# Performance work log

Hardware: AMD Instinct MI355X
Metric: run time of the kernel (lower is better)

## Reference

```python
import jax, jax.numpy as jnp
import numpy as np

N_NODES = 50000
N_EDGES = 800000
NODE_IN = 5
EDGE_IN = 1
HID = 64


def setup_inputs() -> dict:
    key = jax.random.key(0)
    ks = jax.random.split(key, 16)
    x = jax.random.normal(ks[0], (N_NODES, NODE_IN), dtype=jnp.float32)
    edge_index = jax.random.randint(ks[1], (2, N_EDGES), 0, N_NODES, dtype=jnp.int32)
    edge_attr = jax.random.normal(ks[2], (N_EDGES, EDGE_IN), dtype=jnp.float32)
    def lin(k, fan_in, fan_out):
        b = 1.0 / np.sqrt(fan_in)
        k1, k2 = jax.random.split(k)
        W = jax.random.uniform(k1, (fan_in, fan_out), minval=-b, maxval=b, dtype=jnp.float32)
        bi = jax.random.uniform(k2, (fan_out,), minval=-b, maxval=b, dtype=jnp.float32)
        return W, bi
    W_ne, b_ne = lin(ks[3], NODE_IN, HID)
    W_ee, b_ee = lin(ks[4], EDGE_IN, HID)
    W_gcn, b_gcn = lin(ks[5], HID, HID)   # PyG GCNConv: lin (no bias) + separate bias
    W1, b1 = lin(ks[6], 3 * HID, HID)
    W2, b2 = lin(ks[7], HID, 1)
    return {"x": x, "edge_index": edge_index, "edge_attr": edge_attr,
            "W_ne": W_ne, "b_ne": b_ne, "W_ee": W_ee, "b_ee": b_ee,
            "W_gcn": W_gcn, "b_gcn": b_gcn, "W1": W1, "b1": b1, "W2": W2, "b2": b2}


def gcn_conv(h, edge_index, W, b):
    # PyG GCNConv: add self-loops, symmetric norm D^-1/2 (A+I) D^-1/2, linear, scatter-add.
    N = h.shape[0]
    src, dst = edge_index[0], edge_index[1]
    loops = jnp.arange(N, dtype=src.dtype)
    row = jnp.concatenate([src, loops])  # message sources
    col = jnp.concatenate([dst, loops])  # message targets
    deg = jax.ops.segment_sum(jnp.ones(col.shape[0], h.dtype), col, num_segments=N)
    dinv = jnp.where(deg > 0, jax.lax.rsqrt(deg), 0.0)
    norm = dinv[row] * dinv[col]          # [E+N]
    ht = h @ W                            # [N, HID]
    msg = ht[row] * norm[:, None]         # gather + scale
    return jax.ops.segment_sum(msg, col, num_segments=N) + b


def reference(x, edge_index, edge_attr, W_ne, b_ne, W_ee, b_ee, W_gcn, b_gcn, W1, b1, W2, b2):
    h = jax.nn.relu(x @ W_ne + b_ne)                    # node encoder
    ef = jax.nn.relu(edge_attr @ W_ee + b_ee)           # edge encoder
    h = gcn_conv(h, edge_index, W_gcn, b_gcn)           # GCN layer
    src, dst = edge_index[0], edge_index[1]
    edge_input = jnp.concatenate([h[src], h[dst], ef], axis=1)  # [E, 3*HID]
    out = jax.nn.relu(edge_input @ W1 + b1) @ W2 + b2   # edge MLP -> [E, 1]
    return out.reshape(-1)
```

## Files before the change

kernel.cpp:

```cpp
#include <hip/hip_runtime.h>

#define NN 50000
#define NE 800000
#define H  64
#define NBKT 196
#define BCAP 8192
#define BIN_CHUNK 2048

typedef __attribute__((ext_vector_type(8))) short bf16x8;
typedef __attribute__((ext_vector_type(4))) float f32x4;

__device__ __forceinline__ unsigned short f2bf(float f) {
  unsigned int u = __builtin_bit_cast(unsigned int, f);
  u += 0x7FFFu + ((u >> 16) & 1u);
  return (unsigned short)(u >> 16);
}
__device__ __forceinline__ float bf2f(unsigned short u) {
  unsigned int v = ((unsigned int)u) << 16;
  return __builtin_bit_cast(float, v);
}

__global__ __launch_bounds__(256) void k_prep(
    const float* __restrict__ W1, const float* __restrict__ b1,
    const float* __restrict__ W_ee, const float* __restrict__ b_ee,
    float* __restrict__ thrS, float* __restrict__ cT,
    unsigned short* __restrict__ w1f, int* __restrict__ gcur) {
  const int t = threadIdx.x;
  if (blockIdx.x == 2) {
    if (t < NBKT) gcur[t] = 0;
    return;
  }
  if (blockIdx.x == 1) {
    const int ln = t & 63, q = t >> 6;
    const int l15_ = ln & 15, l4_ = ln >> 4;
#pragma unroll
    for (int f = 0; f < 4; ++f) {
      const int idx = q * 4 + f;
      const int g = idx >> 3;
      const int ct = (idx >> 1) & 3;
      const int c = idx & 1;
#pragma unroll
      for (int j = 0; j < 8; ++j) {
        const int k = g * 64 + c * 32 + l4_ * 8 + j;
        const int hcol = ct * 16 + l15_;
        w1f[(idx * 64 + ln) * 8 + j] = f2bf(W1[k * H + hcol]);
      }
    }
    return;
  }
  __shared__ float swee[64], sbee[64], sth[64];
  __shared__ int skx[64];
  if (t < 64) {
    const float w = W_ee[t], b = b_ee[t];
    swee[t] = w; sbee[t] = b;
    sth[t] = (w != 0.f) ? (-b / w) : __builtin_inff();
    skx[t] = t;
  }
  __syncthreads();
  for (int sz = 2; sz <= 64; sz <<= 1)
    for (int st = sz >> 1; st > 0; st >>= 1) {
      if (t < 64) {
        const int p = t ^ st;
        if (p > t) {
          const bool up = ((t & sz) == 0);
          const float a = sth[t], bb = sth[p];
          if (up ? (a > bb) : (a < bb)) {
            const int ka = skx[t];
            sth[t] = bb; sth[p] = a;
            skx[t] = skx[p]; skx[p] = ka;
          }
        }
      }
      __syncthreads();
    }
  if (t < 64) {
    const int h = t;
    float c1 = 0.f, c0 = b1[h];
    for (int k = 0; k < 64; ++k) {
      const float w = swee[k], b = sbee[k];
      if (w < 0.f || (w == 0.f && b > 0.f)) {
        const float wv1 = W1[(128 + k) * H + h];
        c1 = fmaf(w, wv1, c1);
        c0 = fmaf(b, wv1, c0);
      }
    }
    float2* cT2 = (float2*)cT;
    cT2[h] = make_float2(c1, c0);
    for (int iv = 1; iv <= 64; ++iv) {
      const int ks = skx[iv - 1];
      const float w = swee[ks];
      const float s = (w > 0.f) ? 1.f : -1.f;
      const float wv1 = W1[(128 + ks) * H + h];
      c1 = fmaf(s * w, wv1, c1);
      c0 = fmaf(s * sbee[ks], wv1, c0);
      cT2[iv * 66 + h] = make_float2(c1, c0);
    }
    thrS[h] = sth[h];
  }
}

__global__ __launch_bounds__(256) void k_bin(const int* __restrict__ ei,
                                             unsigned int* __restrict__ gbin,
                                             int* __restrict__ gcur) {
  __shared__ int hist[NBKT], base[NBKT];
  const int t = threadIdx.x;
  if (t < NBKT) hist[t] = 0;
  __syncthreads();

  const int e0 = blockIdx.x * BIN_CHUNK;
  int srcv[8], dstv[8], loff[8];
#pragma unroll
  for (int j = 0; j < 8; ++j) {
    const int e = e0 + j * 256 + t;
    if (e < NE) {
      srcv[j] = ei[e];
      dstv[j] = ei[NE + e];
      loff[j] = atomicAdd(&hist[dstv[j] >> 8], 1);
    } else dstv[j] = -1;
  }
  __syncthreads();
  if (t < NBKT) base[t] = atomicAdd(&gcur[t], hist[t]);
  __syncthreads();
#pragma unroll
  for (int j = 0; j < 8; ++j) {
    if (dstv[j] >= 0) {
      const int b = dstv[j] >> 8;
      const int pos = base[b] + loff[j];
      if (pos < BCAP)
        gbin[(size_t)b * BCAP + pos] =
            ((unsigned int)srcv[j] << 8) | (unsigned int)(dstv[j] & 255);
    }
  }
}

__global__ __launch_bounds__(256) void k_pass2(const unsigned int* __restrict__ gbin,
                                               const int* __restrict__ gcur,
                                               unsigned short* __restrict__ gcsr,
                                               int2* __restrict__ rowrange,
                                               float* __restrict__ dinv) {
  __shared__ int hist[256], cur[256], sc[256];
  __shared__ unsigned short lcsr[BCAP];
  const int b = blockIdx.x, t = threadIdx.x;
  const int sz = min(gcur[b], BCAP);
  hist[t] = 0;
  __syncthreads();

  const unsigned int* bb = gbin + (size_t)b * BCAP;
  for (int i = t; i < sz; i += 256) atomicAdd(&hist[bb[i] & 255], 1);
  __syncthreads();

  int v = hist[t];
  const int cnt = v;
  sc[t] = v;
  __syncthreads();
#pragma unroll
  for (int off = 1; off < 256; off <<= 1) {
    const int o = (t >= off) ? sc[t - off] : 0;
    __syncthreads();
    v += o;
    sc[t] = v;
    __syncthreads();
  }
  const int ex = v - cnt;
  cur[t] = ex;
  const int d = b * 256 + t;
  if (d < NN) {
    const int beg = b * BCAP + ex;
    rowrange[d] = make_int2(beg, beg + cnt);
    dinv[d] = rsqrtf((float)(cnt + 1));
  }
  __syncthreads();

  for (int i = t; i < sz; i += 256) {
    const unsigned int en = bb[i];
    const int off = atomicAdd(&cur[en & 255], 1);
    lcsr[off] = (unsigned short)(en >> 8);
  }
  __syncthreads();
  for (int i = t; i < sz; i += 256) gcsr[(size_t)b * BCAP + i] = lcsr[i];
}

__global__ __launch_bounds__(256) void k_node(
    const float* __restrict__ x, const float* __restrict__ W_ne,
    const float* __restrict__ b_ne, const float* __restrict__ W_gcn,
    const float* __restrict__ dinv, unsigned short* __restrict__ htb) {
  __shared__ float sh[4][H];
  const int lane = threadIdx.x & 63;
  const int wv   = threadIdx.x >> 6;
  const int n    = blockIdx.x * 4 + wv;

  float acc = b_ne[lane];
#pragma unroll
  for (int k = 0; k < 5; ++k) acc = fmaf(x[n * 5 + k], W_ne[k * H + lane], acc);
  acc = fmaxf(acc, 0.0f);
  sh[wv][lane] = acc;
  __syncthreads();

  float hv = 0.0f;
#pragma unroll 8
  for (int k = 0; k < H; ++k) hv = fmaf(sh[wv][k], W_gcn[k * H + lane], hv);

  htb[(size_t)n * H + lane] = f2bf(hv * dinv[n]);
}

__global__ __launch_bounds__(256) void k_gather_uv(
    const int2* __restrict__ rowrange, const unsigned short* __restrict__ gcsr,
    const unsigned short* __restrict__ htb, const float* __restrict__ dinv,
    const float* __restrict__ b_gcn, const unsigned short* __restrict__ w1f,
    unsigned short* __restrict__ u, unsigned short* __restrict__ v) {
  __shared__ unsigned short shg[16 * 64];
  const int lane = threadIdx.x & 63;
  const int wv   = threadIdx.x >> 6;
  const int n0   = blockIdx.x * 16;
  const float bg = b_gcn[lane];

#pragma unroll 1
  for (int q = 0; q < 4; ++q) {
    const int nl = wv * 4 + q;
    const int n  = n0 + nl;
    const int2 rr = rowrange[n];
    float sum = bf2f(htb[(size_t)n * H + lane]);
    int i = rr.x;
#pragma unroll 1
    for (; i + 4 <= rr.y; i += 4) {
      const int s0 = gcsr[i], s1 = gcsr[i + 1];
      const int s2 = gcsr[i + 2], s3 = gcsr[i + 3];
      const float v0 = bf2f(htb[(size_t)s0 * H + lane]);
      const float v1 = bf2f(htb[(size_t)s1 * H + lane]);
      const float v2 = bf2f(htb[(size_t)s2 * H + lane]);
      const float v3 = bf2f(htb[(size_t)s3 * H + lane]);
      sum += (v0 + v1) + (v2 + v3);
    }
#pragma unroll 1
    for (; i < rr.y; ++i) sum += bf2f(htb[(size_t)gcsr[i] * H + lane]);

    const float hgv = fmaf(dinv[n], sum, bg);
    shg[((nl * 128 + lane * 2) ^ ((nl & 7) << 4)) >> 1] = f2bf(hgv);
  }
  __syncthreads();

  const int l15 = lane & 15, l4 = lane >> 4;
  const bf16x8 a0 = *(const bf16x8*)(shg + (((l15 * 128 + l4 * 16) ^ ((l15 & 7) << 4)) >> 1));
  const bf16x8 a1 = *(const bf16x8*)(shg + (((l15 * 128 + 64 + l4 * 16) ^ ((l15 & 7) << 4)) >> 1));

  const int ct = wv;
  const bf16x8 bu0 = *(const bf16x8*)(w1f + ((ct * 2 + 0) * 64 + lane) * 8);
  const bf16x8 bu1 = *(const bf16x8*)(w1f + ((ct * 2 + 1) * 64 + lane) * 8);
  const bf16x8 bv0 = *(const bf16x8*)(w1f + ((8 + ct * 2 + 0) * 64 + lane) * 8);
  const bf16x8 bv1 = *(const bf16x8*)(w1f + ((8 + ct * 2 + 1) * 64 + lane) * 8);

  f32x4 au = (f32x4)(0.f), av = (f32x4)(0.f);
  au = __builtin_amdgcn_mfma_f32_16x16x32_bf16(a0, bu0, au, 0, 0, 0);
  au = __builtin_amdgcn_mfma_f32_16x16x32_bf16(a1, bu1, au, 0, 0, 0);
  av = __builtin_amdgcn_mfma_f32_16x16x32_bf16(a0, bv0, av, 0, 0, 0);
  av = __builtin_amdgcn_mfma_f32_16x16x32_bf16(a1, bv1, av, 0, 0, 0);

#pragma unroll
  for (int r = 0; r < 4; ++r) {
    const size_t idx = (size_t)(n0 + l4 * 4 + r) * H + ct * 16 + l15;
    u[idx] = f2bf(au[r]);
    v[idx] = f2bf(av[r]);
  }
}

__device__ __forceinline__ int find_iv(const float* __restrict__ sThr, float ea) {
  int iv = 0;
#pragma unroll
  for (int st = 64; st >= 1; st >>= 1) {
    const int nc = iv + st;
    if (nc <= 64 && sThr[nc - 1] <= ea) iv = nc;
  }
  return iv;
}

__device__ __forceinline__ void edge_compute(
    float ea, uint4 U0, uint4 U1, uint4 V0, uint4 V1,
    const float* __restrict__ sThr, const float* __restrict__ sCT,
    const float* __restrict__ w2v, int l4, int lane, float b2v,
    float* __restrict__ out, int obase) {
  const int iv = find_iv(sThr, ea);
  const float* cp = sCT + iv * 132 + l4 * 32;
  const unsigned int ud[8] = {U0.x, U0.y, U0.z, U0.w, U1.x, U1.y, U1.z, U1.w};
  const unsigned int vd[8] = {V0.x, V0.y, V0.z, V0.w, V1.x, V1.y, V1.z, V1.w};
  float p = 0.f;
#pragma unroll
  for (int r = 0; r < 8; ++r) {
    const float4 cc = *(const float4*)(cp + r * 4);
    const float ulo = __builtin_bit_cast(float, ud[r] << 16);
    const float uhi = __builtin_bit_cast(float, ud[r] & 0xFFFF0000u);
    const float vlo = __builtin_bit_cast(float, vd[r] << 16);
    const float vhi = __builtin_bit_cast(float, vd[r] & 0xFFFF0000u);
    const float z0 = ulo + vlo + fmaf(ea, cc.x, cc.y);
    const float z1 = uhi + vhi + fmaf(ea, cc.z, cc.w);
    p = fmaf(fmaxf(z0, 0.f), w2v[2 * r], p);
    p = fmaf(fmaxf(z1, 0.f), w2v[2 * r + 1], p);
  }
  p += __shfl_xor(p, 16);
  p += __shfl_xor(p, 32);
  if (lane < 16) out[obase + lane] = p + b2v;
}

#define ET 5
__global__ __launch_bounds__(256) void k_edge(
    const int* __restrict__ ei, const float* __restrict__ eattr,
    const unsigned short* __restrict__ u, const unsigned short* __restrict__ v,
    const float* __restrict__ thrS, const float* __restrict__ cT,
    const float* __restrict__ W2, const float* __restrict__ b2,
    float* __restrict__ out) {
  __shared__ float sThr[64];
  __shared__ float sCT[65 * 132];

  const int t = threadIdx.x;
  if (t < 64) sThr[t] = thrS[t];
  for (int i = t; i < 65 * 66; i += 256)
    ((float2*)sCT)[i] = ((const float2*)cT)[i];
  __syncthreads();

  const int lane = t & 63;
  const int wv   = t >> 6;
  const int l15  = lane & 15, l4 = lane >> 4;
  const float b2v = b2[0];

  float w2v[16];
#pragma unroll
  for (int j = 0; j < 16; ++j) w2v[j] = W2[l4 * 16 + j];

  const int tile0 = (blockIdx.x * 4 + wv) * ET;
  int srcA[ET], dstA[ET];
  float eaA[ET];
#pragma unroll
  for (int tt = 0; tt < ET; ++tt) {
    srcA[tt] = ei[(tile0 + tt) * 16 + l15];
    dstA[tt] = ei[NE + (tile0 + tt) * 16 + l15];
    eaA[tt]  = eattr[(tile0 + tt) * 16 + l15];
  }

  uint4 Au0, Au1, Av0, Av1, Bu0, Bu1, Bv0, Bv1;

#define LOADUV(U0, U1, V0, V1, tt) {                              \
    const unsigned short* up = u + (size_t)srcA[tt] * H + l4 * 16; \
    const unsigned short* vp = v + (size_t)dstA[tt] * H + l4 * 16; \
    U0 = *(const uint4*)(up); U1 = *(const uint4*)(up + 8);        \
    V0 = *(const uint4*)(vp); V1 = *(const uint4*)(vp + 8); }

  LOADUV(Au0, Au1, Av0, Av1, 0);
  LOADUV(Bu0, Bu1, Bv0, Bv1, 1);
  edge_compute(eaA[0], Au0, Au1, Av0, Av1, sThr, sCT, w2v, l4, lane, b2v, out, (tile0 + 0) * 16);
  LOADUV(Au0, Au1, Av0, Av1, 2);
  edge_compute(eaA[1], Bu0, Bu1, Bv0, Bv1, sThr, sCT, w2v, l4, lane, b2v, out, (tile0 + 1) * 16);
  LOADUV(Bu0, Bu1, Bv0, Bv1, 3);
  edge_compute(eaA[2], Au0, Au1, Av0, Av1, sThr, sCT, w2v, l4, lane, b2v, out, (tile0 + 2) * 16);
  LOADUV(Au0, Au1, Av0, Av1, 4);
  edge_compute(eaA[3], Bu0, Bu1, Bv0, Bv1, sThr, sCT, w2v, l4, lane, b2v, out, (tile0 + 3) * 16);
  edge_compute(eaA[4], Au0, Au1, Av0, Av1, sThr, sCT, w2v, l4, lane, b2v, out, (tile0 + 4) * 16);
#undef LOADUV
}

extern "C" void kernel_launch(void* const* d_in, const int* in_sizes, int n_in,
                              void* d_out, int out_size, void* d_ws, size_t ws_size,
                              hipStream_t stream) {
  const float* x     = (const float*)d_in[0];
  const int*   ei    = (const int*)d_in[1];
  const float* eattr = (const float*)d_in[2];
  const float* W_ne  = (const float*)d_in[3];
  const float* b_ne  = (const float*)d_in[4];
  const float* W_ee  = (const float*)d_in[5];
  const float* b_ee  = (const float*)d_in[6];
  const float* W_gcn = (const float*)d_in[7];
  const float* b_gcn = (const float*)d_in[8];
  const float* W1    = (const float*)d_in[9];
  const float* b1    = (const float*)d_in[10];
  const float* W2    = (const float*)d_in[11];
  const float* b2    = (const float*)d_in[12];
  float* out = (float*)d_out;

  char* ws = (char*)d_ws;
  unsigned short* htb = (unsigned short*)(ws + 0);
  unsigned short* uT  = (unsigned short*)(ws + 6400000);
  unsigned int*   gbin = (unsigned int*)(ws + 12800000);
  unsigned short* vT  = (unsigned short*)(ws + 12800000);
  unsigned short* gcsr = (unsigned short*)(ws + 19222528);
  int2*  rowrange = (int2*)(ws + 22433792);
  float* dinv    = (float*)(ws + 22833792);
  int*   gcur    = (int*)(ws + 23033792);
  float* thrS    = (float*)(ws + 23034592);
  float* cT      = (float*)(ws + 23034848);
  unsigned short* w1f = (unsigned short*)(ws + 23069168);

  k_prep<<<3, 256, 0, stream>>>(W1, b1, W_ee, b_ee, thrS, cT, w1f, gcur);
  k_bin<<<(NE + BIN_CHUNK - 1) / BIN_CHUNK, 256, 0, stream>>>(ei, gbin, gcur);
  k_pass2<<<NBKT, 256, 0, stream>>>(gbin, gcur, gcsr, rowrange, dinv);
  k_node<<<NN / 4, 256, 0, stream>>>(x, W_ne, b_ne, W_gcn, dinv, htb);
  k_gather_uv<<<NN / 16, 256, 0, stream>>>(rowrange, gcsr, htb, dinv, b_gcn, w1f, uT, vT);
  k_edge<<<NE / (4 * ET * 16), 256, 0, stream>>>(ei, eattr, uT, vT, thrS, cT, W2, b2, out);
}
```

Baseline: 159.4 us.

## Replace CSR build and gather with bucket-wise LDS atomic aggregation

Removes the per-bucket CSR sorting kernel. Node degrees are now counted with global atomics during binning. The gather kernel is replaced by one 1024-thread block per destination bucket, which scatter-adds neighbour features into a shared-memory accumulator with LDS float atomics and then runs the W1 MFMA projection on the 256 rows it owns. This cuts one kernel launch and the CSR write/read traffic. In exchange it adds global atomic contention, uses only 196 large blocks with a large LDS footprint that limits occupancy, and still overlays the v output on the bin buffer.

```diff
diff --git a/kernel.cpp b/kernel.cpp
--- a/kernel.cpp
+++ b/kernel.cpp
@@ -24,10 +24,13 @@
     const float* __restrict__ W1, const float* __restrict__ b1,
     const float* __restrict__ W_ee, const float* __restrict__ b_ee,
     float* __restrict__ thrS, float* __restrict__ cT,
-    unsigned short* __restrict__ w1f, int* __restrict__ gcur) {
+    unsigned short* __restrict__ w1f, int* __restrict__ cnt,
+    int* __restrict__ gcur) {
   const int t = threadIdx.x;
-  if (blockIdx.x == 2) {
-    if (t < NBKT) gcur[t] = 0;
+  if (blockIdx.x >= 2) {
+    const int i = (blockIdx.x - 2) * 256 + t;
+    if (i < NN) cnt[i] = 0;
+    if (blockIdx.x == 2 && t < NBKT) gcur[t] = 0;
     return;
   }
   if (blockIdx.x == 1) {
@@ -101,7 +104,8 @@
 
 __global__ __launch_bounds__(256) void k_bin(const int* __restrict__ ei,
                                              unsigned int* __restrict__ gbin,
-                                             int* __restrict__ gcur) {
+                                             int* __restrict__ gcur,
+                                             int* __restrict__ cnt) {
   __shared__ int hist[NBKT], base[NBKT];
   const int t = threadIdx.x;
   if (t < NBKT) hist[t] = 0;
@@ -116,6 +120,7 @@
       srcv[j] = ei[e];
       dstv[j] = ei[NE + e];
       loff[j] = atomicAdd(&hist[dstv[j] >> 8], 1);
+      atomicAdd(&cnt[dstv[j]], 1);
     } else dstv[j] = -1;
   }
   __syncthreads();
@@ -133,57 +138,10 @@
   }
 }
 
-__global__ __launch_bounds__(256) void k_pass2(const unsigned int* __restrict__ gbin,
-                                               const int* __restrict__ gcur,
-                                               unsigned short* __restrict__ gcsr,
-                                               int2* __restrict__ rowrange,
-                                               float* __restrict__ dinv) {
-  __shared__ int hist[256], cur[256], sc[256];
-  __shared__ unsigned short lcsr[BCAP];
-  const int b = blockIdx.x, t = threadIdx.x;
-  const int sz = min(gcur[b], BCAP);
-  hist[t] = 0;
-  __syncthreads();
-
-  const unsigned int* bb = gbin + (size_t)b * BCAP;
-  for (int i = t; i < sz; i += 256) atomicAdd(&hist[bb[i] & 255], 1);
-  __syncthreads();
-
-  int v = hist[t];
-  const int cnt = v;
-  sc[t] = v;
-  __syncthreads();
-#pragma unroll
-  for (int off = 1; off < 256; off <<= 1) {
-    const int o = (t >= off) ? sc[t - off] : 0;
-    __syncthreads();
-    v += o;
-    sc[t] = v;
-    __syncthreads();
-  }
-  const int ex = v - cnt;
-  cur[t] = ex;
-  const int d = b * 256 + t;
-  if (d < NN) {
-    const int beg = b * BCAP + ex;
-    rowrange[d] = make_int2(beg, beg + cnt);
-    dinv[d] = rsqrtf((float)(cnt + 1));
-  }
-  __syncthreads();
-
-  for (int i = t; i < sz; i += 256) {
-    const unsigned int en = bb[i];
-    const int off = atomicAdd(&cur[en & 255], 1);
-    lcsr[off] = (unsigned short)(en >> 8);
-  }
-  __syncthreads();
-  for (int i = t; i < sz; i += 256) gcsr[(size_t)b * BCAP + i] = lcsr[i];
-}
-
 __global__ __launch_bounds__(256) void k_node(
     const float* __restrict__ x, const float* __restrict__ W_ne,
     const float* __restrict__ b_ne, const float* __restrict__ W_gcn,
-    const float* __restrict__ dinv, unsigned short* __restrict__ htb) {
+    const int* __restrict__ cnt, unsigned short* __restrict__ htb) {
   __shared__ float sh[4][H];
   const int lane = threadIdx.x & 63;
   const int wv   = threadIdx.x >> 6;
@@ -200,66 +158,79 @@
 #pragma unroll 8
   for (int k = 0; k < H; ++k) hv = fmaf(sh[wv][k], W_gcn[k * H + lane], hv);
 
-  htb[(size_t)n * H + lane] = f2bf(hv * dinv[n]);
-}
-
-__global__ __launch_bounds__(256) void k_gather_uv(
-    const int2* __restrict__ rowrange, const unsigned short* __restrict__ gcsr,
-    const unsigned short* __restrict__ htb, const float* __restrict__ dinv,
+  const float dv = rsqrtf((float)(cnt[n] + 1));
+  htb[(size_t)n * H + lane] = f2bf(hv * dv);
+}
+
+__global__ __launch_bounds__(1024) void k_agg(
+    const unsigned int* __restrict__ gbin, const int* __restrict__ gcur,
+    const int* __restrict__ cnt, const unsigned short* __restrict__ htb,
     const float* __restrict__ b_gcn, const unsigned short* __restrict__ w1f,
     unsigned short* __restrict__ u, unsigned short* __restrict__ v) {
-  __shared__ unsigned short shg[16 * 64];
-  const int lane = threadIdx.x & 63;
-  const int wv   = threadIdx.x >> 6;
-  const int n0   = blockIdx.x * 16;
-  const float bg = b_gcn[lane];
-
-#pragma unroll 1
-  for (int q = 0; q < 4; ++q) {
-    const int nl = wv * 4 + q;
-    const int n  = n0 + nl;
-    const int2 rr = rowrange[n];
-    float sum = bf2f(htb[(size_t)n * H + lane]);
-    int i = rr.x;
-#pragma unroll 1
-    for (; i + 4 <= rr.y; i += 4) {
-      const int s0 = gcsr[i], s1 = gcsr[i + 1];
-      const int s2 = gcsr[i + 2], s3 = gcsr[i + 3];
-      const float v0 = bf2f(htb[(size_t)s0 * H + lane]);
-      const float v1 = bf2f(htb[(size_t)s1 * H + lane]);
-      const float v2 = bf2f(htb[(size_t)s2 * H + lane]);
-      const float v3 = bf2f(htb[(size_t)s3 * H + lane]);
-      sum += (v0 + v1) + (v2 + v3);
-    }
-#pragma unroll 1
-    for (; i < rr.y; ++i) sum += bf2f(htb[(size_t)gcsr[i] * H + lane]);
-
-    const float hgv = fmaf(dinv[n], sum, bg);
-    shg[((nl * 128 + lane * 2) ^ ((nl & 7) << 4)) >> 1] = f2bf(hgv);
+  __shared__ float sacc[256 * 66];
+  const int b = blockIdx.x;
+  const int t = threadIdx.x;
+  const int lane = t & 63, wv = t >> 6;
+
+#pragma unroll
+  for (int i = 0; i < 16; ++i) {
+    const int r = wv + i * 16;
+    const int d = b * 256 + r;
+    sacc[r * 66 + lane] = (d < NN) ? bf2f(htb[(size_t)d * H + lane]) : 0.f;
+  }
+  __syncthreads();
+
+  const int sz = min(gcur[b], BCAP);
+  const unsigned int* bb = gbin + (size_t)b * BCAP;
+  int i = wv;
+  for (; i + 16 < sz; i += 32) {
+    const unsigned int e0 = bb[i], e1 = bb[i + 16];
+    const float h0 = bf2f(htb[(size_t)(e0 >> 8) * H + lane]);
+    const float h1 = bf2f(htb[(size_t)(e1 >> 8) * H + lane]);
+    atomicAdd(&sacc[(int)(e0 & 255) * 66 + lane], h0);
+    atomicAdd(&sacc[(int)(e1 & 255) * 66 + lane], h1);
+  }
+  if (i < sz) {
+    const unsigned int e0 = bb[i];
+    const float h0 = bf2f(htb[(size_t)(e0 >> 8) * H + lane]);
+    atomicAdd(&sacc[(int)(e0 & 255) * 66 + lane], h0);
   }
   __syncthreads();
 
   const int l15 = lane & 15, l4 = lane >> 4;
-  const bf16x8 a0 = *(const bf16x8*)(shg + (((l15 * 128 + l4 * 16) ^ ((l15 & 7) << 4)) >> 1));
-  const bf16x8 a1 = *(const bf16x8*)(shg + (((l15 * 128 + 64 + l4 * 16) ^ ((l15 & 7) << 4)) >> 1));
-
-  const int ct = wv;
-  const bf16x8 bu0 = *(const bf16x8*)(w1f + ((ct * 2 + 0) * 64 + lane) * 8);
-  const bf16x8 bu1 = *(const bf16x8*)(w1f + ((ct * 2 + 1) * 64 + lane) * 8);
-  const bf16x8 bv0 = *(const bf16x8*)(w1f + ((8 + ct * 2 + 0) * 64 + lane) * 8);
-  const bf16x8 bv1 = *(const bf16x8*)(w1f + ((8 + ct * 2 + 1) * 64 + lane) * 8);
-
-  f32x4 au = (f32x4)(0.f), av = (f32x4)(0.f);
-  au = __builtin_amdgcn_mfma_f32_16x16x32_bf16(a0, bu0, au, 0, 0, 0);
-  au = __builtin_amdgcn_mfma_f32_16x16x32_bf16(a1, bu1, au, 0, 0, 0);
-  av = __builtin_amdgcn_mfma_f32_16x16x32_bf16(a0, bv0, av, 0, 0, 0);
-  av = __builtin_amdgcn_mfma_f32_16x16x32_bf16(a1, bv1, av, 0, 0, 0);
-
-#pragma unroll
-  for (int r = 0; r < 4; ++r) {
-    const size_t idx = (size_t)(n0 + l4 * 4 + r) * H + ct * 16 + l15;
-    u[idx] = f2bf(au[r]);
-    v[idx] = f2bf(av[r]);
+  const int rowl = wv * 16 + l15;
+  const int nA = b * 256 + rowl;
+  const float dv = (nA < NN) ? rsqrtf((float)(cnt[nA] + 1)) : 0.f;
+
+  bf16x8 a0, a1;
+#pragma unroll
+  for (int j = 0; j < 8; ++j) {
+    a0[j] = (short)f2bf(fmaf(dv, sacc[rowl * 66 + l4 * 8 + j], b_gcn[l4 * 8 + j]));
+    a1[j] = (short)f2bf(fmaf(dv, sacc[rowl * 66 + 32 + l4 * 8 + j], b_gcn[32 + l4 * 8 + j]));
+  }
+
+#pragma unroll
+  for (int ct = 0; ct < 4; ++ct) {
+    const bf16x8 bu0 = *(const bf16x8*)(w1f + ((ct * 2 + 0) * 64 + lane) * 8);
+    const bf16x8 bu1 = *(const bf16x8*)(w1f + ((ct * 2 + 1) * 64 + lane) * 8);
+    const bf16x8 bv0 = *(const bf16x8*)(w1f + ((8 + ct * 2 + 0) * 64 + lane) * 8);
+    const bf16x8 bv1 = *(const bf16x8*)(w1f + ((8 + ct * 2 + 1) * 64 + lane) * 8);
+
+    f32x4 au = (f32x4)(0.f), av = (f32x4)(0.f);
+    au = __builtin_amdgcn_mfma_f32_16x16x32_bf16(a0, bu0, au, 0, 0, 0);
+    au = __builtin_amdgcn_mfma_f32_16x16x32_bf16(a1, bu1, au, 0, 0, 0);
+    av = __builtin_amdgcn_mfma_f32_16x16x32_bf16(a0, bv0, av, 0, 0, 0);
+    av = __builtin_amdgcn_mfma_f32_16x16x32_bf16(a1, bv1, av, 0, 0, 0);
+
+#pragma unroll
+    for (int r = 0; r < 4; ++r) {
+      const int nn = b * 256 + wv * 16 + l4 * 4 + r;
+      if (nn < NN) {
+        const size_t idx = (size_t)nn * H + ct * 16 + l15;
+        u[idx] = f2bf(au[r]);
+        v[idx] = f2bf(av[r]);
+      }
+    }
   }
 }
 
@@ -379,18 +350,15 @@
   unsigned short* uT  = (unsigned short*)(ws + 6400000);
   unsigned int*   gbin = (unsigned int*)(ws + 12800000);
   unsigned short* vT  = (unsigned short*)(ws + 12800000);
-  unsigned short* gcsr = (unsigned short*)(ws + 19222528);
-  int2*  rowrange = (int2*)(ws + 22433792);
-  float* dinv    = (float*)(ws + 22833792);
-  int*   gcur    = (int*)(ws + 23033792);
-  float* thrS    = (float*)(ws + 23034592);
-  float* cT      = (float*)(ws + 23034848);
-  unsigned short* w1f = (unsigned short*)(ws + 23069168);
-
-  k_prep<<<3, 256, 0, stream>>>(W1, b1, W_ee, b_ee, thrS, cT, w1f, gcur);
-  k_bin<<<(NE + BIN_CHUNK - 1) / BIN_CHUNK, 256, 0, stream>>>(ei, gbin, gcur);
-  k_pass2<<<NBKT, 256, 0, stream>>>(gbin, gcur, gcsr, rowrange, dinv);
-  k_node<<<NN / 4, 256, 0, stream>>>(x, W_ne, b_ne, W_gcn, dinv, htb);
-  k_gather_uv<<<NN / 16, 256, 0, stream>>>(rowrange, gcsr, htb, dinv, b_gcn, w1f, uT, vT);
+  int*   cnt     = (int*)(ws + 19222528);
+  int*   gcur    = (int*)(ws + 19422528);
+  float* thrS    = (float*)(ws + 19423328);
+  float* cT      = (float*)(ws + 19423584);
+  unsigned short* w1f = (unsigned short*)(ws + 19457904);
+
+  k_prep<<<2 + NBKT, 256, 0, stream>>>(W1, b1, W_ee, b_ee, thrS, cT, w1f, cnt, gcur);
+  k_bin<<<(NE + BIN_CHUNK - 1) / BIN_CHUNK, 256, 0, stream>>>(ei, gbin, gcur, cnt);
+  k_node<<<NN / 4, 256, 0, stream>>>(x, W_ne, b_ne, W_gcn, cnt, htb);
+  k_agg<<<NBKT, 1024, 0, stream>>>(gbin, gcur, cnt, htb, b_gcn, w1f, uT, vT);
   k_edge<<<NE / (4 * ET * 16), 256, 0, stream>>>(ei, eattr, uT, vT, thrS, cT, W2, b2, out);
 }
```

New measurement: 494.6 us. +210.3%, slower.
